# Optimization experiments

Hardware: AMD Instinct MI355X
Metric: run time of the kernel (lower is better)

The kernel has to match this reference:

```python
import jax, jax.numpy as jnp
import numpy as np

EMBED_DIM = 1024
HEAD_DIM = 128
SEQ = 2048
BATCH = 16


def setup_inputs() -> dict:
    key = jax.random.key(0)
    ks = jax.random.split(key, 7)
    s = 1.0 / np.sqrt(EMBED_DIM)
    return {
        "x": jax.random.normal(ks[0], (BATCH, SEQ, EMBED_DIM), dtype=jnp.float32),
        "Wq": jax.random.uniform(ks[1], (EMBED_DIM, HEAD_DIM), jnp.float32, -s, s),
        "bq": jax.random.uniform(ks[2], (HEAD_DIM,), jnp.float32, -s, s),
        "Wk": jax.random.uniform(ks[3], (EMBED_DIM, HEAD_DIM), jnp.float32, -s, s),
        "bk": jax.random.uniform(ks[4], (HEAD_DIM,), jnp.float32, -s, s),
        "Wv": jax.random.uniform(ks[5], (EMBED_DIM, HEAD_DIM), jnp.float32, -s, s),
        "bv": jax.random.uniform(ks[6], (HEAD_DIM,), jnp.float32, -s, s),
    }


def reference(x, Wq, bq, Wk, bk, Wv, bv):
    # q,k,v: [B,S,Dh]
    q = x @ Wq + bq
    k = x @ Wk + bk
    v = x @ Wv + bv
    # NOTE: original module MULTIPLIES by embed_dim**0.5 (faithful to source).
    scale = jnp.asarray(EMBED_DIM ** 0.5, dtype=x.dtype)
    scores = jnp.einsum("bqd,bkd->bqk", q, k) * scale  # [B,S,S]
    causal = jnp.tril(jnp.ones((SEQ, SEQ), dtype=bool))
    scores = jnp.where(causal, scores, -jnp.inf)
    attn = jax.nn.softmax(scores, axis=-1)
    # dropout_rate=0 -> identity
    return jnp.einsum("bqk,bkd->bqd", attn, v)
```

## Files before the change

### kernel.cpp

```cpp
#include <hip/hip_runtime.h>

#define BATCH 16
#define SEQ   2048
#define EMB   1024
#define DH    128

typedef _Float16 half4_t __attribute__((ext_vector_type(4)));
typedef _Float16 half8_t __attribute__((ext_vector_type(8)));
typedef float    f32x4   __attribute__((ext_vector_type(4)));

#define OFF_WT2 0u
#define OFF_QHI 0x200000u
#define OFF_QLO (OFF_QHI + 0x800000u)
#define OFF_KHI (OFF_QLO + 0x800000u)
#define OFF_KLO (OFF_KHI + 0x800000u)
#define OFF_VT  (OFF_KLO + 0x800000u)

__device__ __forceinline__ void gload16(const void* g, void* l) {
    __builtin_amdgcn_global_load_lds(
        (__attribute__((address_space(1))) const unsigned int*)g,
        (__attribute__((address_space(3))) unsigned int*)l, 16, 0, 0);
}

__global__ __launch_bounds__(256) void prep_w(
    const float* __restrict__ Wq, const float* __restrict__ Wk,
    const float* __restrict__ Wv, _Float16* __restrict__ Wt2) {
    const int t  = blockIdx.x * 256 + threadIdx.x;
    const int kc = t / 2560, rem = t % 2560;
    const int lo = rem >= 1536 ? 1 : 0;
    const int rr = lo ? rem - 1536 : rem;
    const int nt = rr >> 6, c = rr & 63;
    const int g = c >> 4, r = c & 15;
    const int k0 = kc * 32 + g * 8;
    const float* W; int col;
    if (nt < 8)       { W = Wq; col = nt * 16 + r; }
    else if (nt < 16) { W = Wk; col = (nt - 8) * 16 + r; }
    else              { W = Wv; col = (nt - 16) * 16 + r; }
    half8_t v;
#pragma unroll
    for (int j = 0; j < 8; ++j) {
        float f = W[(size_t)(k0 + j) * DH + col];
        _Float16 h = (_Float16)f;
        v[j] = lo ? (_Float16)(f - (float)h) : h;
    }
    *(half8_t*)((char*)Wt2 + (size_t)kc * 40960 + (lo ? 24576 : 0)
                + (size_t)nt * 1024 + c * 16) = v;
}

#define XBUF  0
#define WBUF  32768
#define FHI   114688
#define FLO   122880

__global__ __launch_bounds__(512, 2) void proj_qkv(
    const float* __restrict__ x, const _Float16* __restrict__ Wt2,
    const float* __restrict__ bq, const float* __restrict__ bk,
    const float* __restrict__ bv,
    char* __restrict__ qhi, char* __restrict__ qlo,
    char* __restrict__ khi, char* __restrict__ klo,
    char* __restrict__ vt) {
    __shared__ __align__(16) char lds[131072];
    const int tid = threadIdx.x, lane = tid & 63, w = tid >> 6;
    const int l15 = lane & 15, g = lane >> 4;
    const int m0  = blockIdx.x * 128;

    f32x4 acc[8][3];
#pragma unroll
    for (int mt = 0; mt < 8; ++mt)
#pragma unroll
        for (int j = 0; j < 3; ++j) acc[mt][j] = {};

    auto stage_x = [&](int t, int buf) {
#pragma unroll
        for (int i = 0; i < 2; ++i) {
            const int cb = w * 128 + i * 64;
            const int sidx = cb + lane;
            const int r = sidx >> 3, s = sidx & 7;
            const int c = s ^ (r & 7);
            gload16(x + (size_t)(m0 + r) * EMB + t * 32 + c * 4,
                    lds + XBUF + buf * 16384 + cb * 16);
        }
    };

    auto stage_w = [&](int t, int buf) {
        const char* wsrc = (const char*)Wt2 + (size_t)t * 40960;
#pragma unroll
        for (int i = 0; i < 5; ++i) {
            const int off = (w * 5 + i) * 1024;
            gload16(wsrc + off + lane * 16, lds + WBUF + buf * 40960 + off);
        }
    };

    auto compute = [&](int buf) {
        const char* wb = lds + WBUF + buf * 40960;
        half8_t qh = *(const half8_t*)(wb + (size_t)w * 1024 + lane * 16);
        half8_t ql = *(const half8_t*)(wb + 24576 + (size_t)w * 1024 + lane * 16);
        half8_t kh = *(const half8_t*)(wb + (size_t)(8 + w) * 1024 + lane * 16);
        half8_t kl = *(const half8_t*)(wb + 24576 + (size_t)(8 + w) * 1024 + lane * 16);
        half8_t vh = *(const half8_t*)(wb + (size_t)(16 + w) * 1024 + lane * 16);
#pragma unroll
        for (int mt = 0; mt < 8; ++mt) {
            const int RR = mt * 16 + l15;
            const int sl = (g ^ ((RR >> 1) & 3)) * 16;
            half8_t xh = *(const half8_t*)(lds + FHI + RR * 64 + sl);
            half8_t xl = *(const half8_t*)(lds + FLO + RR * 64 + sl);
            acc[mt][0] = __builtin_amdgcn_mfma_f32_16x16x32_f16(xh, qh, acc[mt][0], 0, 0, 0);
            acc[mt][0] = __builtin_amdgcn_mfma_f32_16x16x32_f16(xl, qh, acc[mt][0], 0, 0, 0);
            acc[mt][0] = __builtin_amdgcn_mfma_f32_16x16x32_f16(xh, ql, acc[mt][0], 0, 0, 0);
            acc[mt][1] = __builtin_amdgcn_mfma_f32_16x16x32_f16(xh, kh, acc[mt][1], 0, 0, 0);
            acc[mt][1] = __builtin_amdgcn_mfma_f32_16x16x32_f16(xl, kh, acc[mt][1], 0, 0, 0);
            acc[mt][1] = __builtin_amdgcn_mfma_f32_16x16x32_f16(xh, kl, acc[mt][1], 0, 0, 0);
            acc[mt][2] = __builtin_amdgcn_mfma_f32_16x16x32_f16(xh, vh, acc[mt][2], 0, 0, 0);
        }
    };

    stage_x(0, 0);
    stage_w(0, 0);

    for (int t = 0; t < 32; ++t) {
        __syncthreads();

        {
            const char* Xb = lds + XBUF + (t & 1) * 16384;
            const int R = tid >> 2;
            const int s = tid & 3;
            const int rx = R & 7;
            f32x4 a0 = *(const f32x4*)(Xb + R * 128 + ((2 * s)     ^ rx) * 16);
            f32x4 a1 = *(const f32x4*)(Xb + R * 128 + ((2 * s + 1) ^ rx) * 16);
            half8_t hi, lo;
#pragma unroll
            for (int jj = 0; jj < 4; ++jj) {
                float f = a0[jj]; _Float16 h = (_Float16)f;
                hi[jj] = h; lo[jj] = (_Float16)(f - (float)h);
                float f2 = a1[jj]; _Float16 h2 = (_Float16)f2;
                hi[jj + 4] = h2; lo[jj + 4] = (_Float16)(f2 - (float)h2);
            }
            const int sw = (s ^ ((R >> 1) & 3)) * 16;
            *(half8_t*)(lds + FHI + R * 64 + sw) = hi;
            *(half8_t*)(lds + FLO + R * 64 + sw) = lo;
        }
        __syncthreads();

        if (t < 31) {
            stage_x(t + 1, (t + 1) & 1);
            stage_w(t + 1, (t + 1) & 1);
        }
        __builtin_amdgcn_sched_barrier(0);

        compute(t & 1);
    }

    __syncthreads();
    float* scr = (float*)(lds + (size_t)w * 1280);
    const float SC = 46.166241308446828f;

#pragma unroll
    for (int j = 0; j < 3; ++j) {
        float bias;
        if (j == 0)      bias = bq[w * 16 + l15];
        else if (j == 1) bias = bk[w * 16 + l15];
        else             bias = bv[w * 16 + l15];
#pragma unroll
        for (int mt = 0; mt < 8; ++mt) {
            f32x4 a = acc[mt][j];
#pragma unroll
            for (int r = 0; r < 4; ++r) {
                float v = a[r] + bias;
                if (j == 0) v *= SC;
                scr[(g * 4 + r) * 20 + l15] = v;
            }
            if (j < 2) {
                f32x4 tv = *(const f32x4*)(scr + l15 * 20 + g * 4);
                half4_t h4, l4;
#pragma unroll
                for (int r = 0; r < 4; ++r) {
                    _Float16 h = (_Float16)tv[r];
                    h4[r] = h; l4[r] = (_Float16)(tv[r] - (float)h);
                }
                const int tIdx = blockIdx.x * 8 + mt;
                const int octm = 2 * w + (g >> 1);
                const size_t off = (size_t)tIdx * 4096 + (octm >> 2) * 1024
                                 + (octm & 3) * 256 + l15 * 16 + (g & 1) * 8;
                char* dh_ = (j == 0) ? qhi : khi;
                char* dl_ = (j == 0) ? qlo : klo;
                *(half4_t*)(dh_ + off) = h4;
                *(half4_t*)(dl_ + off) = l4;
            } else {
                half4_t v4;
#pragma unroll
                for (int r = 0; r < 4; ++r)
                    v4[r] = (_Float16)scr[(g * 4 + r) * 20 + l15];
                const int s0 = (m0 & (SEQ - 1)) + mt * 16;
                const int b  = m0 >> 11;
                const size_t off = ((size_t)b * 64 + (s0 >> 5)) * 8192
                                 + ((s0 >> 4) & 1) * 4096 + (size_t)w * 512
                                 + g * 128 + l15 * 8;
                *(half4_t*)(vt + off) = v4;
            }
        }
    }
}

__global__ __launch_bounds__(512) void attn(
    const char* __restrict__ qhi, const char* __restrict__ qlo,
    const char* __restrict__ khi, const char* __restrict__ klo,
    const char* __restrict__ vt, float* __restrict__ out) {
    __shared__ __align__(16) char lds[49152];
    const int tid = threadIdx.x, lane = tid & 63, w = tid >> 6;
    const int l15 = lane & 15, g = lane >> 4;
    const int gid = blockIdx.x;
    const int b   = ((gid & 7) << 1) | ((gid >> 3) & 1);
    const int pr  = gid >> 4;
    const int jt  = (w < 4) ? (31 - pr) : pr;
    const int wq  = w & 3;
    const int qw0 = jt * 64 + wq * 16;
    const int nkv = 2 * (32 - pr);

    auto stage = [&](int t, int buf) {
        char* dst = lds + buf * 24576;
        const size_t kb4 = ((size_t)b * 128 + t * 2) * 4096;
        const size_t vb8 = ((size_t)b * 64 + t) * 8192;
        const int off = w * 1024;
        gload16(khi + kb4 + off + lane * 16, dst + off);
        gload16(klo + kb4 + off + lane * 16, dst + 8192 + off);
        gload16(vt  + vb8 + off + lane * 16, dst + 16384 + off);
    };

    const size_t qt4 = ((size_t)b * 128 + (qw0 >> 4)) * 4096;
    half8_t Qh[4], Ql[4];
#pragma unroll
    for (int kk = 0; kk < 4; ++kk) {
        const size_t o = qt4 + kk * 1024 + g * 256 + l15 * 16;
        Qh[kk] = *(const half8_t*)(qhi + o);
        Ql[kk] = *(const half8_t*)(qlo + o);
    }

    f32x4 o[8];
#pragma unroll
    for (int dt = 0; dt < 8; ++dt) o[dt] = {};
    float mrun = -3.0e38f, ell = 0.0f;

    stage(0, 0);

    for (int t = 0; t < nkv; ++t) {
        __syncthreads();
        if (t + 1 < nkv) stage(t + 1, (t + 1) & 1);

        const int kb = t * 32;
        if (kb <= qw0 + 15) {
            const char* kbuf = lds + (t & 1) * 24576;

            f32x4 sa0 = {}, sb0 = {}, sa1 = {}, sb1 = {};
            __builtin_amdgcn_s_setprio(1);
#pragma unroll
            for (int kk = 0; kk < 4; ++kk) {
                const int fo = kk * 1024 + g * 256 + l15 * 16;
                half8_t kh0 = *(const half8_t*)(kbuf + fo);
                half8_t kl0 = *(const half8_t*)(kbuf + 8192 + fo);
                half8_t kh1 = *(const half8_t*)(kbuf + 4096 + fo);
                half8_t kl1 = *(const half8_t*)(kbuf + 12288 + fo);
                sa0 = __builtin_amdgcn_mfma_f32_16x16x32_f16(kh0, Qh[kk], sa0, 0, 0, 0);
                sb0 = __builtin_amdgcn_mfma_f32_16x16x32_f16(kl0, Qh[kk], sb0, 0, 0, 0);
                sb0 = __builtin_amdgcn_mfma_f32_16x16x32_f16(kh0, Ql[kk], sb0, 0, 0, 0);
                sa1 = __builtin_amdgcn_mfma_f32_16x16x32_f16(kh1, Qh[kk], sa1, 0, 0, 0);
                sb1 = __builtin_amdgcn_mfma_f32_16x16x32_f16(kl1, Qh[kk], sb1, 0, 0, 0);
                sb1 = __builtin_amdgcn_mfma_f32_16x16x32_f16(kh1, Ql[kk], sb1, 0, 0, 0);
            }
            __builtin_amdgcn_s_setprio(0);
            f32x4 s0 = sa0 + sb0, s1 = sa1 + sb1;

            if (kb + 31 > qw0) {
#pragma unroll
                for (int r = 0; r < 4; ++r) {
                    if (kb + g * 4 + r      > qw0 + l15) s0[r] = -3.0e38f;
                    if (kb + 16 + g * 4 + r > qw0 + l15) s1[r] = -3.0e38f;
                }
            }

            float mt = fmaxf(fmaxf(fmaxf(s0[0], s0[1]), fmaxf(s0[2], s0[3])),
                             fmaxf(fmaxf(s1[0], s1[1]), fmaxf(s1[2], s1[3])));
            mt = fmaxf(mt, __shfl_xor(mt, 16, 64));
            mt = fmaxf(mt, __shfl_xor(mt, 32, 64));
            if (!__all(mt <= mrun + 8.0f)) {
                const float mnew = fmaxf(mrun, mt);
                const float alpha = exp2f(mrun - mnew);
                ell *= alpha;
#pragma unroll
                for (int dt = 0; dt < 8; ++dt) o[dt] *= alpha;
                mrun = mnew;
            }
            float p[8];
#pragma unroll
            for (int r = 0; r < 4; ++r) {
                p[r]     = exp2f(s0[r] - mrun);
                p[4 + r] = exp2f(s1[r] - mrun);
            }
            float ps = ((p[0] + p[1]) + (p[2] + p[3])) + ((p[4] + p[5]) + (p[6] + p[7]));
            ps += __shfl_xor(ps, 16, 64);
            ps += __shfl_xor(ps, 32, 64);
            ell += ps;

            half4_t pf0, pf1;
#pragma unroll
            for (int r = 0; r < 4; ++r) { pf0[r] = (_Float16)p[r]; pf1[r] = (_Float16)p[4 + r]; }

            const char* vbuf = kbuf + 16384;
            __builtin_amdgcn_s_setprio(1);
#pragma unroll
            for (int dt = 0; dt < 8; ++dt) {
                const int vo = dt * 512 + g * 128 + l15 * 8;
                half4_t v0 = *(const half4_t*)(vbuf + vo);
                half4_t v1 = *(const half4_t*)(vbuf + 4096 + vo);
                o[dt] = __builtin_amdgcn_mfma_f32_16x16x16f16(v0, pf0, o[dt], 0, 0, 0);
                o[dt] = __builtin_amdgcn_mfma_f32_16x16x16f16(v1, pf1, o[dt], 0, 0, 0);
            }
            __builtin_amdgcn_s_setprio(0);
        }
    }

    const float rinv = 1.0f / ell;
    float* orow = out + ((size_t)b * SEQ + qw0 + l15) * DH + g * 4;
#pragma unroll
    for (int dt = 0; dt < 8; ++dt) {
        f32x4 ov = o[dt] * rinv;
        *(f32x4*)(orow + dt * 16) = ov;
    }
}

extern "C" void kernel_launch(void* const* d_in, const int* in_sizes, int n_in,
                              void* d_out, int out_size, void* d_ws, size_t ws_size,
                              hipStream_t stream) {
    const float* x  = (const float*)d_in[0];
    const float* Wq = (const float*)d_in[1];
    const float* bq = (const float*)d_in[2];
    const float* Wk = (const float*)d_in[3];
    const float* bk = (const float*)d_in[4];
    const float* Wv = (const float*)d_in[5];
    const float* bv = (const float*)d_in[6];
    float* out = (float*)d_out;

    char* ws = (char*)d_ws;
    _Float16* Wt2 = (_Float16*)(ws + OFF_WT2);
    char* q_hi = ws + OFF_QHI;
    char* q_lo = ws + OFF_QLO;
    char* k_hi = ws + OFF_KHI;
    char* k_lo = ws + OFF_KLO;
    char* v_t  = ws + OFF_VT;

    prep_w  <<<320, 256, 0, stream>>>(Wq, Wk, Wv, Wt2);
    proj_qkv<<<256, 512, 0, stream>>>(x, Wt2, bq, bk, bv, q_hi, q_lo, k_hi, k_lo, v_t);
    attn    <<<256, 512, 0, stream>>>(q_hi, q_lo, k_hi, k_lo, v_t, out);
}
```

Baseline: 140.0 us.

## Load projection weights directly from global and defer softmax row-sum reduction

The projection kernel stops staging the weight tiles through LDS and has each wave read its weight fragments straight from global memory (L2-resident). This shrinks LDS per block from 128KB to 48KB and raises the launch-bounds occupancy hint from 2 to 4 blocks. In the attention kernel, the per-tile cross-lane shuffle reduction of the softmax denominator is replaced by per-lane accumulation with a single reduction at the end. The risk is exposed global-load latency inside the MFMA loop, since the weight loads are no longer prefetched.

```diff
diff --git a/kernel.cpp b/kernel.cpp
--- a/kernel.cpp
+++ b/kernel.cpp
@@ -48,18 +48,17 @@
 }
 
 #define XBUF  0
-#define WBUF  32768
-#define FHI   114688
-#define FLO   122880
-
-__global__ __launch_bounds__(512, 2) void proj_qkv(
+#define FHI   32768
+#define FLO   40960
+
+__global__ __launch_bounds__(512, 4) void proj_qkv(
     const float* __restrict__ x, const _Float16* __restrict__ Wt2,
     const float* __restrict__ bq, const float* __restrict__ bk,
     const float* __restrict__ bv,
     char* __restrict__ qhi, char* __restrict__ qlo,
     char* __restrict__ khi, char* __restrict__ klo,
     char* __restrict__ vt) {
-    __shared__ __align__(16) char lds[131072];
+    __shared__ __align__(16) char lds[49152];
     const int tid = threadIdx.x, lane = tid & 63, w = tid >> 6;
     const int l15 = lane & 15, g = lane >> 4;
     const int m0  = blockIdx.x * 128;
@@ -82,22 +81,13 @@
         }
     };
 
-    auto stage_w = [&](int t, int buf) {
-        const char* wsrc = (const char*)Wt2 + (size_t)t * 40960;
-#pragma unroll
-        for (int i = 0; i < 5; ++i) {
-            const int off = (w * 5 + i) * 1024;
-            gload16(wsrc + off + lane * 16, lds + WBUF + buf * 40960 + off);
-        }
-    };
-
-    auto compute = [&](int buf) {
-        const char* wb = lds + WBUF + buf * 40960;
-        half8_t qh = *(const half8_t*)(wb + (size_t)w * 1024 + lane * 16);
-        half8_t ql = *(const half8_t*)(wb + 24576 + (size_t)w * 1024 + lane * 16);
-        half8_t kh = *(const half8_t*)(wb + (size_t)(8 + w) * 1024 + lane * 16);
-        half8_t kl = *(const half8_t*)(wb + 24576 + (size_t)(8 + w) * 1024 + lane * 16);
-        half8_t vh = *(const half8_t*)(wb + (size_t)(16 + w) * 1024 + lane * 16);
+    auto compute = [&](int t) {
+        const char* wp = (const char*)Wt2 + (size_t)t * 40960 + lane * 16;
+        half8_t qh = *(const half8_t*)(wp + (size_t)w * 1024);
+        half8_t ql = *(const half8_t*)(wp + 24576 + (size_t)w * 1024);
+        half8_t kh = *(const half8_t*)(wp + (size_t)(8 + w) * 1024);
+        half8_t kl = *(const half8_t*)(wp + 24576 + (size_t)(8 + w) * 1024);
+        half8_t vh = *(const half8_t*)(wp + (size_t)(16 + w) * 1024);
 #pragma unroll
         for (int mt = 0; mt < 8; ++mt) {
             const int RR = mt * 16 + l15;
@@ -115,7 +105,6 @@
     };
 
     stage_x(0, 0);
-    stage_w(0, 0);
 
     for (int t = 0; t < 32; ++t) {
         __syncthreads();
@@ -141,13 +130,10 @@
         }
         __syncthreads();
 
-        if (t < 31) {
-            stage_x(t + 1, (t + 1) & 1);
-            stage_w(t + 1, (t + 1) & 1);
-        }
+        if (t < 31) stage_x(t + 1, (t + 1) & 1);
         __builtin_amdgcn_sched_barrier(0);
 
-        compute(t & 1);
+        compute(t);
     }
 
     __syncthreads();
@@ -295,10 +281,7 @@
                 p[r]     = exp2f(s0[r] - mrun);
                 p[4 + r] = exp2f(s1[r] - mrun);
             }
-            float ps = ((p[0] + p[1]) + (p[2] + p[3])) + ((p[4] + p[5]) + (p[6] + p[7]));
-            ps += __shfl_xor(ps, 16, 64);
-            ps += __shfl_xor(ps, 32, 64);
-            ell += ps;
+            ell += ((p[0] + p[1]) + (p[2] + p[3])) + ((p[4] + p[5]) + (p[6] + p[7]));
 
             half4_t pf0, pf1;
 #pragma unroll
@@ -317,6 +300,9 @@
             __builtin_amdgcn_s_setprio(0);
         }
     }
+
+    ell += __shfl_xor(ell, 16, 64);
+    ell += __shfl_xor(ell, 32, 64);
 
     const float rinv = 1.0f / ell;
     float* orow = out + ((size_t)b * SEQ + qw0 + l15) * DH + g * 4;
```

Measured after the change: 184.6 us. 31.9% more time.
